# Kernel tuning notes

Hardware: AMD Instinct MI355X
Metric: run time of the kernel (lower is better)

## Reference

```python
import jax, jax.numpy as jnp
import numpy as np

N = 16384
H = 256
C = 2


def setup_inputs() -> dict:
    key = jax.random.key(0)
    ks = jax.random.split(key, 9)
    s = lambda fan_in: 1.0 / np.sqrt(fan_in)
    return {
        "coordinates": jax.random.normal(ks[0], (N, C), dtype=jnp.float32) * 10.0,
        "W1": jax.random.normal(ks[1], (C, H), dtype=jnp.float32) * s(C),
        "b1": jnp.zeros((H,), dtype=jnp.float32),
        "W2": jax.random.normal(ks[2], (H, H), dtype=jnp.float32) * s(H),
        "b2": jnp.zeros((H,), dtype=jnp.float32),
        "Wd1": jax.random.normal(ks[3], (1, H // 2), dtype=jnp.float32) * s(1),
        "bd1": jnp.zeros((H // 2,), dtype=jnp.float32),
        "Wd2": jax.random.normal(ks[4], (H // 2, H), dtype=jnp.float32) * s(H // 2),
        "bd2": jnp.zeros((H,), dtype=jnp.float32),
        "k": 6,
    }


def reference(coordinates, W1, b1, W2, b2, Wd1, bd1, Wd2, bd2, k):
    x = coordinates.astype(jnp.float32)
    # coord MLP: Linear -> SiLU -> Linear
    coord_emb = jax.nn.silu(x @ W1 + b1) @ W2 + b2  # (N, H)

    # pairwise Euclidean distances (N, N), via ||a||^2 + ||b||^2 - 2ab
    sq = jnp.sum(x * x, axis=1)  # (N,)
    d2 = sq[:, None] + sq[None, :] - 2.0 * (x @ x.T)
    dist = jnp.sqrt(jnp.maximum(d2, 1e-12))  # safe sqrt; diag ~ 0

    # k+1 smallest distances per row (includes self at ~0), ascending
    kk = min(k + 1, dist.shape[1])
    neg_top, _ = jax.lax.top_k(-dist, kk)
    topk_dist = -neg_top  # ascending smallest
    mean_dist = jnp.mean(topk_dist[:, 1:], axis=1, keepdims=True)  # (N, 1)

    dist_emb = jax.nn.silu(mean_dist @ Wd1 + bd1) @ Wd2 + bd2  # (N, H)
    return coord_emb + dist_emb
```

## Files before the change

kernel.cpp:

```cpp
#include <hip/hip_runtime.h>
#include <float.h>
#include <math.h>

#define NPTS 16384
#define HDIM 256

#define KNB   256
#define KXMIN (-48.0f)
#define KW    0.375f
#define KINVW (1.0f / KW)

typedef __attribute__((ext_vector_type(8))) short bf16x8;
typedef __attribute__((ext_vector_type(4))) float f32x4;

__device__ __forceinline__ float silu_f(float z) {
    return z / (1.0f + __expf(-z));
}

__device__ __forceinline__ short f2bf(float f) {
    unsigned u = __float_as_uint(f);
    u = (u + 0x7FFFu + ((u >> 16) & 1u)) >> 16;
    return (short)u;
}

__device__ __forceinline__ float bcast_lane(float x, int l) {
    return __int_as_float(__builtin_amdgcn_readlane(__float_as_int(x), l));
}

__device__ __forceinline__ int binof(float x) {
    int b = (int)floorf((x - KXMIN) * KINVW);
    return b < 0 ? 0 : (b > KNB - 1 ? KNB - 1 : b);
}

__global__ void zero_kernel(unsigned* __restrict__ hist) {
    hist[threadIdx.x] = 0u;
}

__global__ __launch_bounds__(256) void hist_kernel(const float* __restrict__ xyf,
                                                   unsigned* __restrict__ hist) {
    __shared__ unsigned lh[KNB];
    lh[threadIdx.x] = 0u;
    __syncthreads();
    for (int i = blockIdx.x * 256 + threadIdx.x; i < NPTS; i += gridDim.x * 256)
        atomicAdd(&lh[binof(xyf[2 * i])], 1u);
    __syncthreads();
    const unsigned c = lh[threadIdx.x];
    if (c) atomicAdd(&hist[threadIdx.x], c);
}

__global__ __launch_bounds__(256) void scan_kernel(const unsigned* __restrict__ hist,
                                                   unsigned* __restrict__ off,
                                                   unsigned* __restrict__ cursor) {
    __shared__ unsigned sh[KNB];
    const int tid = threadIdx.x;
    const unsigned own = hist[tid];
    sh[tid] = own;
    __syncthreads();
    for (int s = 1; s < KNB; s <<= 1) {
        const unsigned v = (tid >= s) ? sh[tid - s] : 0u;
        __syncthreads();
        sh[tid] += v;
        __syncthreads();
    }
    const unsigned excl = sh[tid] - own;
    off[tid]    = excl;
    cursor[tid] = excl;
    if (tid == KNB - 1) off[KNB] = (unsigned)NPTS;
}

__global__ __launch_bounds__(256) void scatter_kernel(const float* __restrict__ xyf,
                                                      unsigned* __restrict__ cursor,
                                                      float2* __restrict__ sxy) {
    for (int i = blockIdx.x * 256 + threadIdx.x; i < NPTS; i += gridDim.x * 256) {
        const float2 p = ((const float2*)xyf)[i];
        const unsigned pos = atomicAdd(&cursor[binof(p.x)], 1u);
        sxy[pos] = p;
    }
}

__global__ __launch_bounds__(512, 8) void knn_search(const float* __restrict__ xyf,
                                                     const float2* __restrict__ sxy,
                                                     const unsigned* __restrict__ off,
                                                     float* __restrict__ md) {
    const int lane = threadIdx.x & 63;
    const int qid  = blockIdx.x * 8 + (threadIdx.x >> 6);
    const float2 q = ((const float2*)xyf)[qid];

    float s0 = FLT_MAX, s1 = FLT_MAX, s2 = FLT_MAX, s3 = FLT_MAX,
          s4 = FLT_MAX, s5 = FLT_MAX, s6 = FLT_MAX;

    auto process = [&](int bb) {
        const unsigned o = off[bb], e = off[bb + 1];
        for (unsigned base = o; base < e; base += 64) {
            const unsigned idx = base + lane;
            float d2 = FLT_MAX;
            if (idx < e) {
                const float2 p = sxy[idx];
                const float dx = q.x - p.x, dy = q.y - p.y;
                d2 = fmaf(dx, dx, dy * dy);
            }
            unsigned long long m = __ballot(d2 < s6);
            while (m) {
                const int L  = __ffsll(m) - 1;
                const float v = bcast_lane(d2, L);
                s6 = fmaxf(s5, v);
                s5 = fmaxf(s4, fminf(s5, v));
                s4 = fmaxf(s3, fminf(s4, v));
                s3 = fmaxf(s2, fminf(s3, v));
                s2 = fmaxf(s1, fminf(s2, v));
                s1 = fmaxf(s0, fminf(s1, v));
                s0 = fminf(s0, v);
                if (lane == L) d2 = FLT_MAX;
                m = __ballot(d2 < s6);
            }
        }
    };

    const int b0 = binof(q.x);
    process(b0);
    int l = b0 - 1, r = b0 + 1;
    while (l >= 0 || r < KNB) {
        float bl = FLT_MAX, br = FLT_MAX;
        if (l >= 0) {
            const float d = fmaxf(q.x - (KXMIN + (float)(l + 1) * KW), 0.0f);
            bl = d * d;
        }
        if (r < KNB) {
            const float d = fmaxf((KXMIN + (float)r * KW) - q.x, 0.0f);
            br = d * d;
        }
        if (fminf(bl, br) > s6) break;
        if (bl <= br) { process(l); --l; }
        else          { process(r); ++r; }
    }

    if (lane == 0) {
        const float sum = sqrtf(fmaxf(s1, 1e-12f)) + sqrtf(fmaxf(s2, 1e-12f)) +
                          sqrtf(fmaxf(s3, 1e-12f)) + sqrtf(fmaxf(s4, 1e-12f)) +
                          sqrtf(fmaxf(s5, 1e-12f)) + sqrtf(fmaxf(s6, 1e-12f));
        md[qid] = sum * (1.0f / 6.0f);
    }
}

__global__ __launch_bounds__(256) void pack_kernel(const float* __restrict__ W2,
                                                   const float* __restrict__ Wd2,
                                                   unsigned short* __restrict__ W2p,
                                                   unsigned short* __restrict__ Wd2p) {
    const int slot = blockIdx.x * 256 + threadIdx.x;
    const float* src;
    unsigned short* dst;
    int s;
    if (slot < 8192) { src = W2;  dst = W2p;  s = slot; }
    else             { src = Wd2; dst = Wd2p; s = slot - 8192; }
    const int t   = s >> 10;
    const int rem = s & 1023;
    const int ct  = rem >> 6;
    const int l   = rem & 63;
    const int k0  = t * 32 + 8 * (l >> 4);
    const int c   = ct * 16 + (l & 15);
    bf16x8 v;
    #pragma unroll
    for (int i = 0; i < 8; ++i)
        v[i] = f2bf(src[(size_t)(k0 + i) * HDIM + c]);
    ((bf16x8*)dst)[s] = v;
}

#define GEN_A(T)                                                              \
    {                                                                         \
        const int kb = (T) * 32 + klane;                                      \
        const float4 p0 = *(const float4*)(W1 + kb);                          \
        const float4 p1 = *(const float4*)(W1 + kb + 4);                      \
        const float4 r0_ = *(const float4*)(W1 + HDIM + kb);                  \
        const float4 r1_ = *(const float4*)(W1 + HDIM + kb + 4);              \
        const float4 c0_ = *(const float4*)(b1 + kb);                         \
        const float4 c1_ = *(const float4*)(b1 + kb + 4);                     \
        const float pw[8] = {p0.x,p0.y,p0.z,p0.w,p1.x,p1.y,p1.z,p1.w};        \
        const float rw[8] = {r0_.x,r0_.y,r0_.z,r0_.w,r1_.x,r1_.y,r1_.z,r1_.w};\
        const float cw[8] = {c0_.x,c0_.y,c0_.z,c0_.w,c1_.x,c1_.y,c1_.z,c1_.w};\
        _Pragma("unroll")                                                     \
        for (int i = 0; i < 8; ++i)                                           \
            a[i] = f2bf(silu_f(fmaf(q.x, pw[i], fmaf(q.y, rw[i], cw[i]))));   \
    }

#define GEN_G(T)                                                              \
    {                                                                         \
        const int kb = (T) * 32 + klane;                                      \
        const float4 p0 = *(const float4*)(Wd1 + kb);                         \
        const float4 p1 = *(const float4*)(Wd1 + kb + 4);                     \
        const float4 c0_ = *(const float4*)(bd1 + kb);                        \
        const float4 c1_ = *(const float4*)(bd1 + kb + 4);                    \
        const float pw[8] = {p0.x,p0.y,p0.z,p0.w,p1.x,p1.y,p1.z,p1.w};        \
        const float cw[8] = {c0_.x,c0_.y,c0_.z,c0_.w,c1_.x,c1_.y,c1_.z,c1_.w};\
        _Pragma("unroll")                                                     \
        for (int i = 0; i < 8; ++i)                                           \
            a[i] = f2bf(silu_f(fmaf(mdr, pw[i], cw[i])));                     \
    }

#define MFMA8(BUF)                                                            \
    _Pragma("unroll")                                                         \
    for (int j = 0; j < 8; ++j)                                               \
        acc[j] = __builtin_amdgcn_mfma_f32_16x16x32_bf16(a, BUF[j], acc[j], 0, 0, 0);

#define LOADB(BUF, ARR, T)                                                    \
    _Pragma("unroll")                                                         \
    for (int j = 0; j < 8; ++j)                                               \
        BUF[j] = ARR[((T) * 16 + ch * 8 + j) * 64 + lane];

__global__ __launch_bounds__(256, 2) void mlp_kernel(
        const float* __restrict__ xyf,
        const float* __restrict__ W1,  const float* __restrict__ b1,
        const float* __restrict__ b2,
        const float* __restrict__ Wd1, const float* __restrict__ bd1,
        const float* __restrict__ bd2,
        const unsigned short* __restrict__ W2p,
        const unsigned short* __restrict__ Wd2p,
        const float* __restrict__ md,  float* __restrict__ out) {
    const int tid  = threadIdx.x;
    const int lane = tid & 63;
    const int w    = tid >> 6;
    const int r0   = blockIdx.x * 32 + (w >> 1) * 16;
    const int ch   = w & 1;
    const int row  = r0 + (lane & 15);
    const float2 q = ((const float2*)xyf)[row];
    const float mdr = md[row];
    const int klane = 8 * (lane >> 4);

    f32x4 acc[8];
    #pragma unroll
    for (int j = 0; j < 8; ++j) {
        acc[j][0] = 0.0f; acc[j][1] = 0.0f; acc[j][2] = 0.0f; acc[j][3] = 0.0f;
    }

    const bf16x8* B1 = (const bf16x8*)W2p;
    const bf16x8* B2 = (const bf16x8*)Wd2p;
    bf16x8 bA[8], bB[8];
    bf16x8 a;

    LOADB(bA, B1, 0)

    #pragma unroll
    for (int tt = 0; tt < 4; ++tt) {
        {   const int t = 2 * tt;
            GEN_A(t)
            LOADB(bB, B1, t + 1)
            MFMA8(bA)
        }
        {   const int t = 2 * tt + 1;
            GEN_A(t)
            if (t + 1 < 8) { LOADB(bA, B1, t + 1) }
            else           { LOADB(bA, B2, 0)     }
            MFMA8(bB)
        }
    }

    #pragma unroll
    for (int uu = 0; uu < 2; ++uu) {
        {   const int t = 2 * uu;
            GEN_G(t)
            LOADB(bB, B2, t + 1)
            MFMA8(bA)
        }
        {   const int t = 2 * uu + 1;
            GEN_G(t)
            if (t + 1 < 4) { LOADB(bA, B2, t + 1) }
            MFMA8(bB)
        }
    }

    const int cb = ch * 128;
    const int rr = r0 + 4 * (lane >> 4);
    #pragma unroll
    for (int j = 0; j < 8; ++j) {
        const int c = cb + j * 16 + (lane & 15);
        const float add = b2[c] + bd2[c];
        out[(size_t)(rr + 0) * HDIM + c] = acc[j][0] + add;
        out[(size_t)(rr + 1) * HDIM + c] = acc[j][1] + add;
        out[(size_t)(rr + 2) * HDIM + c] = acc[j][2] + add;
        out[(size_t)(rr + 3) * HDIM + c] = acc[j][3] + add;
    }
}

extern "C" void kernel_launch(void* const* d_in, const int* in_sizes, int n_in,
                              void* d_out, int out_size, void* d_ws, size_t ws_size,
                              hipStream_t stream) {
    const float* xy  = (const float*)d_in[0];
    const float* W1  = (const float*)d_in[1];
    const float* b1  = (const float*)d_in[2];
    const float* W2  = (const float*)d_in[3];
    const float* b2  = (const float*)d_in[4];
    const float* Wd1 = (const float*)d_in[5];
    const float* bd1 = (const float*)d_in[6];
    const float* Wd2 = (const float*)d_in[7];
    const float* bd2 = (const float*)d_in[8];
    float* out = (float*)d_out;

    char* ws = (char*)d_ws;
    float*          md     = (float*)ws;
    unsigned short* W2p    = (unsigned short*)(ws + 65536);
    unsigned short* Wd2p   = (unsigned short*)(ws + 196608);
    unsigned*       hist   = (unsigned*)(ws + 262144);
    unsigned*       off    = (unsigned*)(ws + 263168);
    unsigned*       cursor = (unsigned*)(ws + 265216);
    float2*         sxy    = (float2*)(ws + 266240);

    zero_kernel<<<1, KNB, 0, stream>>>(hist);
    hist_kernel<<<32, 256, 0, stream>>>(xy, hist);
    scan_kernel<<<1, 256, 0, stream>>>(hist, off, cursor);
    scatter_kernel<<<32, 256, 0, stream>>>(xy, cursor, sxy);
    knn_search<<<NPTS / 8, 512, 0, stream>>>(xy, sxy, off, md);
    pack_kernel<<<48, 256, 0, stream>>>(W2, Wd2, W2p, Wd2p);
    mlp_kernel<<<NPTS / 32, 256, 0, stream>>>(xy, W1, b1, b2, Wd1, bd1, bd2,
                                              W2p, Wd2p, md, out);
}
```

Before: 173.9 us.

## Restructure kNN search to lane-per-query over spatially sorted queries

The kNN search now assigns one query per lane, taking queries from the bin-sorted point array so that each 64-query block covers a narrow x range. Its four waves split the candidate points of each bin, broadcast candidates lane by lane, and merge their top-7 lists through shared memory; results are written back through a saved original-index array. Per-block partial histograms replace the global atomic histogram, which drops the zero kernel. This removes the ballot/serial insertion loop per query-wave, at the cost of block-wide syncs and scanning the union of bins for all 64 queries.

```diff
diff --git a/kernel.cpp b/kernel.cpp
--- a/kernel.cpp
+++ b/kernel.cpp
@@ -9,6 +9,7 @@
 #define KXMIN (-48.0f)
 #define KW    0.375f
 #define KINVW (1.0f / KW)
+#define NHB   32
 
 typedef __attribute__((ext_vector_type(8))) short bf16x8;
 typedef __attribute__((ext_vector_type(4))) float f32x4;
@@ -32,28 +33,25 @@
     return b < 0 ? 0 : (b > KNB - 1 ? KNB - 1 : b);
 }
 
-__global__ void zero_kernel(unsigned* __restrict__ hist) {
-    hist[threadIdx.x] = 0u;
-}
-
 __global__ __launch_bounds__(256) void hist_kernel(const float* __restrict__ xyf,
-                                                   unsigned* __restrict__ hist) {
+                                                   unsigned* __restrict__ histp) {
     __shared__ unsigned lh[KNB];
     lh[threadIdx.x] = 0u;
     __syncthreads();
-    for (int i = blockIdx.x * 256 + threadIdx.x; i < NPTS; i += gridDim.x * 256)
+    for (int i = blockIdx.x * 256 + threadIdx.x; i < NPTS; i += NHB * 256)
         atomicAdd(&lh[binof(xyf[2 * i])], 1u);
     __syncthreads();
-    const unsigned c = lh[threadIdx.x];
-    if (c) atomicAdd(&hist[threadIdx.x], c);
-}
-
-__global__ __launch_bounds__(256) void scan_kernel(const unsigned* __restrict__ hist,
+    histp[blockIdx.x * KNB + threadIdx.x] = lh[threadIdx.x];
+}
+
+__global__ __launch_bounds__(256) void scan_kernel(const unsigned* __restrict__ histp,
                                                    unsigned* __restrict__ off,
                                                    unsigned* __restrict__ cursor) {
     __shared__ unsigned sh[KNB];
     const int tid = threadIdx.x;
-    const unsigned own = hist[tid];
+    unsigned own = 0;
+    #pragma unroll
+    for (int b = 0; b < NHB; ++b) own += histp[b * KNB + tid];
     sh[tid] = own;
     __syncthreads();
     for (int s = 1; s < KNB; s <<= 1) {
@@ -70,75 +68,110 @@
 
 __global__ __launch_bounds__(256) void scatter_kernel(const float* __restrict__ xyf,
                                                       unsigned* __restrict__ cursor,
-                                                      float2* __restrict__ sxy) {
-    for (int i = blockIdx.x * 256 + threadIdx.x; i < NPTS; i += gridDim.x * 256) {
+                                                      float2* __restrict__ sxy,
+                                                      unsigned* __restrict__ qidx) {
+    for (int i = blockIdx.x * 256 + threadIdx.x; i < NPTS; i += NHB * 256) {
         const float2 p = ((const float2*)xyf)[i];
         const unsigned pos = atomicAdd(&cursor[binof(p.x)], 1u);
-        sxy[pos] = p;
-    }
-}
-
-__global__ __launch_bounds__(512, 8) void knn_search(const float* __restrict__ xyf,
-                                                     const float2* __restrict__ sxy,
-                                                     const unsigned* __restrict__ off,
-                                                     float* __restrict__ md) {
+        sxy[pos]  = p;
+        qidx[pos] = (unsigned)i;
+    }
+}
+
+#define LADDER(V)                                   \
+    {   const float v_ = (V);                       \
+        s6 = fmaxf(s5, fminf(s6, v_));              \
+        s5 = fmaxf(s4, fminf(s5, v_));              \
+        s4 = fmaxf(s3, fminf(s4, v_));              \
+        s3 = fmaxf(s2, fminf(s3, v_));              \
+        s2 = fmaxf(s1, fminf(s2, v_));              \
+        s1 = fmaxf(s0, fminf(s1, v_));              \
+        s0 = fminf(s0, v_);                         \
+    }
+
+__global__ __launch_bounds__(256) void knn_search(const float2* __restrict__ sxy,
+                                                  const unsigned* __restrict__ qidx,
+                                                  const unsigned* __restrict__ off,
+                                                  float* __restrict__ md) {
+    __shared__ float mt[64][4][7];
+    __shared__ int wantL, wantR;
+
     const int lane = threadIdx.x & 63;
-    const int qid  = blockIdx.x * 8 + (threadIdx.x >> 6);
-    const float2 q = ((const float2*)xyf)[qid];
+    const int wv   = threadIdx.x >> 6;
+    const int qpos = blockIdx.x * 64 + lane;
+    const float2 q = sxy[qpos];
 
     float s0 = FLT_MAX, s1 = FLT_MAX, s2 = FLT_MAX, s3 = FLT_MAX,
           s4 = FLT_MAX, s5 = FLT_MAX, s6 = FLT_MAX;
 
-    auto process = [&](int bb) {
-        const unsigned o = off[bb], e = off[bb + 1];
-        for (unsigned base = o; base < e; base += 64) {
-            const unsigned idx = base + lane;
-            float d2 = FLT_MAX;
-            if (idx < e) {
-                const float2 p = sxy[idx];
-                const float dx = q.x - p.x, dy = q.y - p.y;
-                d2 = fmaf(dx, dx, dy * dy);
+    auto scan_bin = [&](int b) {
+        const unsigned o = off[b], e = off[b + 1];
+        for (unsigned u = o + 64u * wv; u < e; u += 256u) {
+            const unsigned idx = u + (unsigned)lane;
+            const float2 c = sxy[idx < (unsigned)NPTS ? idx : (unsigned)(NPTS - 1)];
+            const int n = (int)(e - u) < 64 ? (int)(e - u) : 64;
+            for (int j = 0; j < n; ++j) {
+                const float px = bcast_lane(c.x, j);
+                const float py = bcast_lane(c.y, j);
+                const float dx = q.x - px, dy = q.y - py;
+                const float d2 = fmaf(dx, dx, dy * dy);
+                if (d2 < s6) LADDER(d2)
             }
-            unsigned long long m = __ballot(d2 < s6);
-            while (m) {
-                const int L  = __ffsll(m) - 1;
-                const float v = bcast_lane(d2, L);
-                s6 = fmaxf(s5, v);
-                s5 = fmaxf(s4, fminf(s5, v));
-                s4 = fmaxf(s3, fminf(s4, v));
-                s3 = fmaxf(s2, fminf(s3, v));
-                s2 = fmaxf(s1, fminf(s2, v));
-                s1 = fmaxf(s0, fminf(s1, v));
-                s0 = fminf(s0, v);
-                if (lane == L) d2 = FLT_MAX;
-                m = __ballot(d2 < s6);
-            }
         }
     };
 
-    const int b0 = binof(q.x);
-    process(b0);
-    int l = b0 - 1, r = b0 + 1;
-    while (l >= 0 || r < KNB) {
-        float bl = FLT_MAX, br = FLT_MAX;
+    const int bA = binof(bcast_lane(q.x, 0));
+    const int bB = binof(bcast_lane(q.x, 63));
+    for (int b = bA; b <= bB; ++b) scan_bin(b);
+
+    int l = bA - 1, r = bB + 1;
+    if (threadIdx.x == 0) { wantL = 0; wantR = 0; }
+    while (true) {
+        __syncthreads();
+        bool myL = false, myR = false;
         if (l >= 0) {
             const float d = fmaxf(q.x - (KXMIN + (float)(l + 1) * KW), 0.0f);
-            bl = d * d;
+            myL = d * d <= s6;
         }
         if (r < KNB) {
             const float d = fmaxf((KXMIN + (float)r * KW) - q.x, 0.0f);
-            br = d * d;
-        }
-        if (fminf(bl, br) > s6) break;
-        if (bl <= br) { process(l); --l; }
-        else          { process(r); ++r; }
-    }
-
-    if (lane == 0) {
+            myR = d * d <= s6;
+        }
+        if (__ballot(myL) && lane == 0) wantL = 1;
+        if (__ballot(myR) && lane == 0) wantR = 1;
+        __syncthreads();
+        const int wl = wantL, wr = wantR;
+        __syncthreads();
+        if (threadIdx.x == 0) { wantL = 0; wantR = 0; }
+        if (!wl && !wr) break;
+        if (wl) {
+            while (l >= 0 && off[l] == off[l + 1]) --l;
+            if (l >= 0) scan_bin(l);
+            --l;
+        }
+        if (wr) {
+            while (r < KNB && off[r] == off[r + 1]) ++r;
+            if (r < KNB) scan_bin(r);
+            ++r;
+        }
+    }
+
+    mt[lane][wv][0] = s0; mt[lane][wv][1] = s1; mt[lane][wv][2] = s2;
+    mt[lane][wv][3] = s3; mt[lane][wv][4] = s4; mt[lane][wv][5] = s5;
+    mt[lane][wv][6] = s6;
+    __syncthreads();
+    if (wv == 0) {
+        #pragma unroll
+        for (int sl = 1; sl < 4; ++sl)
+            #pragma unroll
+            for (int i = 0; i < 7; ++i) {
+                const float v = mt[lane][sl][i];
+                if (v < s6) LADDER(v)
+            }
         const float sum = sqrtf(fmaxf(s1, 1e-12f)) + sqrtf(fmaxf(s2, 1e-12f)) +
                           sqrtf(fmaxf(s3, 1e-12f)) + sqrtf(fmaxf(s4, 1e-12f)) +
                           sqrtf(fmaxf(s5, 1e-12f)) + sqrtf(fmaxf(s6, 1e-12f));
-        md[qid] = sum * (1.0f / 6.0f);
+        md[qidx[qpos]] = sum * (1.0f / 6.0f);
     }
 }
 
@@ -298,16 +331,16 @@
     float*          md     = (float*)ws;
     unsigned short* W2p    = (unsigned short*)(ws + 65536);
     unsigned short* Wd2p   = (unsigned short*)(ws + 196608);
-    unsigned*       hist   = (unsigned*)(ws + 262144);
-    unsigned*       off    = (unsigned*)(ws + 263168);
-    unsigned*       cursor = (unsigned*)(ws + 265216);
-    float2*         sxy    = (float2*)(ws + 266240);
-
-    zero_kernel<<<1, KNB, 0, stream>>>(hist);
-    hist_kernel<<<32, 256, 0, stream>>>(xy, hist);
-    scan_kernel<<<1, 256, 0, stream>>>(hist, off, cursor);
-    scatter_kernel<<<32, 256, 0, stream>>>(xy, cursor, sxy);
-    knn_search<<<NPTS / 8, 512, 0, stream>>>(xy, sxy, off, md);
+    unsigned*       histp  = (unsigned*)(ws + 262144);
+    unsigned*       off    = (unsigned*)(ws + 294912);
+    unsigned*       cursor = (unsigned*)(ws + 296192);
+    float2*         sxy    = (float2*)(ws + 297216);
+    unsigned*       qidx   = (unsigned*)(ws + 428288);
+
+    hist_kernel<<<NHB, 256, 0, stream>>>(xy, histp);
+    scan_kernel<<<1, 256, 0, stream>>>(histp, off, cursor);
+    scatter_kernel<<<NHB, 256, 0, stream>>>(xy, cursor, sxy, qidx);
+    knn_search<<<NPTS / 64, 256, 0, stream>>>(sxy, qidx, off, md);
     pack_kernel<<<48, 256, 0, stream>>>(W2, Wd2, W2p, Wd2p);
     mlp_kernel<<<NPTS / 32, 256, 0, stream>>>(xy, W1, b1, b2, Wd1, bd1, bd2,
                                               W2p, Wd2p, md, out);
```

Measured after the change: 449.7 us. +158.7%, slower.
